# Kernel optimization log

Hardware: AMD Instinct MI355X
Metric: run time of the kernel (lower is better)

## Reference

```python
import jax, jax.numpy as jnp
import numpy as np


def _conv2d(x, w, stride, padding):
    # x: NCHW, w: OIHW
    return jax.lax.conv_general_dilated(
        x, w, window_strides=(stride, stride),
        padding=((padding, padding), (padding, padding)),
        dimension_numbers=('NCHW', 'OIHW', 'NCHW'))


def setup_inputs() -> dict:
    key = jax.random.key(0)
    k1, k2 = jax.random.split(key)
    B, C_in, H, Wd = 8, 64, 256, 256
    C_out, ksz = 64, 3
    x = jax.random.normal(k1, (B, C_in, H, Wd), dtype=jnp.float32)
    W = jax.random.normal(k2, (C_out, C_in, ksz, ksz), dtype=jnp.float32)
    b = jnp.zeros((C_out,), dtype=jnp.float32)
    return {"x": x, "W": W, "b": b}


def reference(x, W, b):
    stride, padding = 1, 1
    B, C, H, Wd = x.shape
    # per-pixel (across-channel) normalization of activations
    xf = jnp.transpose(x, (0, 2, 3, 1)).reshape(-1, C)       # [B*H*W, C]
    mu = jnp.mean(xf, axis=-1, keepdims=True)
    var = jnp.mean((xf - mu) ** 2, axis=-1, keepdims=True)    # unbiased=False
    r = 1.0 / jnp.sqrt(var + 1e-8)
    y_norm = r * (xf - mu)
    # int8 fake-quant per pixel
    s_act = 127.0 / jnp.maximum(jnp.max(jnp.abs(y_norm), axis=-1, keepdims=True), 1e-8)
    y_tilde = jnp.clip(jnp.round(s_act * y_norm), -128.0, 127.0) / s_act
    y4 = jnp.transpose(y_tilde.reshape(B, H, Wd, C), (0, 3, 1, 2))
    # ternary weight quant (value; STE only matters for backward)
    s_w = 1.0 / jnp.maximum(jnp.mean(jnp.abs(W)), 1e-8)
    w_tilde = jnp.clip(jnp.round(s_w * W), -1.0, 1.0) / s_w
    out = _conv2d(y4, w_tilde, stride, padding) + b[None, :, None, None]
    return out
```

## Files before the change

### kernel.cpp

```cpp
#include <hip/hip_runtime.h>
#include <hip/hip_bf16.h>

typedef _Float16 half8 __attribute__((ext_vector_type(8)));
typedef float    f32x4 __attribute__((ext_vector_type(4)));

#define NB   8
#define NC   64
#define NH   256
#define NW   256
#define NO   64
#define Y_OFF    0ull
#define Y_BYTES  (33554432ull * 2ull)
#define TW_OFF   (Y_OFF + Y_BYTES)
#define TW_BYTES (576ull * 64ull * 2ull)
#define MSW_OFF  (TW_OFF + TW_BYTES)

__global__ __launch_bounds__(256) void wq_kernel(const float* __restrict__ W,
                                                 _Float16* __restrict__ tw2,
                                                 float* __restrict__ msw_out) {
    __shared__ float red[256];
    __shared__ float sw_sh;
    int tid = threadIdx.x;
    float s = 0.0f;
    #pragma unroll
    for (int i = 0; i < 144; ++i) s += fabsf(W[i * 256 + tid]);
    red[tid] = s;
    __syncthreads();
    for (int off = 128; off > 0; off >>= 1) {
        if (tid < off) red[tid] += red[tid + off];
        __syncthreads();
    }
    if (tid == 0) {
        float mean = red[0] / 36864.0f;
        float msw  = fmaxf(mean, 1e-8f);
        sw_sh      = 1.0f / msw;
        msw_out[0] = msw;
    }
    __syncthreads();
    float s_w = sw_sh;
    #pragma unroll
    for (int i = 0; i < 144; ++i) {
        int idx = i * 256 + tid;
        float t = rintf(s_w * W[idx]);
        t = fminf(1.0f, fmaxf(-1.0f, t));
        int o  = idx / 576;
        int r  = idx - o * 576;
        int c  = r / 9;
        int r2 = r - c * 9;
        int kh = r2 / 3;
        int kw = r2 - kh * 3;
        int k  = (kh * 3 + kw) * 64 + c;
        tw2[((k >> 3) * 64 + o) * 8 + (k & 7)] = (_Float16)t;
    }
}

__global__ __launch_bounds__(256, 2) void norm_kernel(const float* __restrict__ x,
                                                      _Float16* __restrict__ y) {
    int p  = blockIdx.x * 256 + threadIdx.x;
    int bb = p >> 16;
    int hw = p & 65535;
    const float* xp = x + (size_t)bb * 64 * 65536 + hw;

    float v[64];
    float s = 0.0f;
    #pragma unroll
    for (int c = 0; c < 64; ++c) { v[c] = xp[(size_t)c * 65536]; s += v[c]; }
    float mu = s * (1.0f / 64.0f);

    float var = 0.0f, dmax = 0.0f;
    #pragma unroll
    for (int c = 0; c < 64; ++c) {
        float d = v[c] - mu;
        var += d * d;
        dmax = fmaxf(dmax, fabsf(d));
    }
    var *= (1.0f / 64.0f);
    float r    = 1.0f / sqrtf(var + 1e-8f);
    float amax = fmaxf(dmax * r, 1e-8f);
    float s_a  = 127.0f / amax;
    float invs = amax / 127.0f;

    half8 hv[8];
    #pragma unroll
    for (int c = 0; c < 64; ++c) {
        float yn = (v[c] - mu) * r;
        float q  = rintf(s_a * yn);
        q = fminf(127.0f, fmaxf(-128.0f, q));
        hv[c >> 3][c & 7] = (_Float16)(q * invs);
    }
    half8* yp = (half8*)(y + (size_t)p * 64);
    #pragma unroll
    for (int j = 0; j < 8; ++j) yp[j] = hv[j];
}

__global__ __launch_bounds__(256, 2) void conv_kernel(const _Float16* __restrict__ y,
                                                      const _Float16* __restrict__ tw2,
                                                      const float* __restrict__ msw_p,
                                                      const float* __restrict__ bias,
                                                      float* __restrict__ out) {
    __shared__ alignas(16) _Float16 lds[3 * 8 * 66 * 8];

    int tid = threadIdx.x;
    int bid = blockIdx.x;
    int wt = bid & 3;
    int h  = (bid >> 2) & 255;
    int bb = bid >> 10;
    int w0 = wt * 64;

    for (int i = tid; i < 1584; i += 256) {
        int cc = i & 7;
        int t8 = i >> 3;
        int wl = t8 % 66;
        int kh = t8 / 66;
        int hp = h + kh - 1;
        int wp = w0 + wl - 1;
        half8 val;
        #pragma unroll
        for (int e = 0; e < 8; ++e) val[e] = (_Float16)0.0f;
        if ((unsigned)hp < 256u && (unsigned)wp < 256u)
            val = *(const half8*)(y + ((((size_t)bb * 256 + hp) * 256 + wp) * 64 + cc * 8));
        *(half8*)(lds + ((kh * 8 + cc) * 66 + wl) * 8) = val;
    }

    int l   = tid & 63;
    int wv  = tid >> 6;
    int l15 = l & 15;
    int q8  = l >> 4;

    half8 aw[18];
    #pragma unroll
    for (int ks = 0; ks < 18; ++ks)
        aw[ks] = *(const half8*)(tw2 + (((ks * 4 + q8) * 64) + wv * 16 + l15) * 8);

    __syncthreads();

    f32x4 acc[4];
    #pragma unroll
    for (int nt = 0; nt < 4; ++nt)
        #pragma unroll
        for (int r2 = 0; r2 < 4; ++r2) acc[nt][r2] = 0.0f;

    #pragma unroll
    for (int ks = 0; ks < 18; ++ks) {
        int tap = ks >> 1;
        int kh  = tap / 3;
        int kw  = tap - kh * 3;
        int ccb = (ks & 1) * 4 + q8;
        int base = ((kh * 8 + ccb) * 66 + kw + l15) * 8;
        #pragma unroll
        for (int nt = 0; nt < 4; ++nt) {
            half8 bf = *(const half8*)(lds + base + nt * 128);
            acc[nt] = __builtin_amdgcn_mfma_f32_16x16x32_f16(aw[ks], bf, acc[nt], 0, 0, 0);
        }
    }

    float msw = *msw_p;
    size_t obase = ((size_t)bb * 64) * 65536 + (size_t)h * 256;
    #pragma unroll
    for (int reg = 0; reg < 4; ++reg) {
        int o = wv * 16 + q8 * 4 + reg;
        float bo = bias[o];
        #pragma unroll
        for (int nt = 0; nt < 4; ++nt) {
            int w = w0 + nt * 16 + l15;
            out[obase + (size_t)o * 65536 + w] = acc[nt][reg] * msw + bo;
        }
    }
}

extern "C" void kernel_launch(void* const* d_in, const int* in_sizes, int n_in,
                              void* d_out, int out_size, void* d_ws, size_t ws_size,
                              hipStream_t stream) {
    const float* x = (const float*)d_in[0];
    const float* W = (const float*)d_in[1];
    const float* b = (const float*)d_in[2];
    float* out = (float*)d_out;

    char* ws = (char*)d_ws;
    _Float16* y   = (_Float16*)(ws + Y_OFF);
    _Float16* tw2 = (_Float16*)(ws + TW_OFF);
    float*    msw = (float*)(ws + MSW_OFF);

    wq_kernel<<<1, 256, 0, stream>>>(W, tw2, msw);
    norm_kernel<<<2048, 256, 0, stream>>>(x, y);
    conv_kernel<<<8192, 256, 0, stream>>>(y, tw2, msw, b, out);
}
```

Before: 315.9 us.

## Compute four output rows per conv block to reuse halo and weight tiles

Each conv block now produces a 4-row by 64-column tile instead of a single row. The input halo grows from 3 to 6 rows shared across the 4 output rows, and each wave holds weights for 32 output channels so each LDS B-fragment feeds two MFMAs. The LDS layout changes to a pixel-major layout padded to 66 halfs per pixel to reduce bank conflicts. The goal is less redundant halo reloading and fewer LDS reads per MFMA, in exchange for more registers (doubled weight fragments and accumulators) and a quarter as many blocks.

```diff
diff --git a/kernel.cpp b/kernel.cpp
--- a/kernel.cpp
+++ b/kernel.cpp
@@ -4,11 +4,6 @@
 typedef _Float16 half8 __attribute__((ext_vector_type(8)));
 typedef float    f32x4 __attribute__((ext_vector_type(4)));
 
-#define NB   8
-#define NC   64
-#define NH   256
-#define NW   256
-#define NO   64
 #define Y_OFF    0ull
 #define Y_BYTES  (33554432ull * 2ull)
 #define TW_OFF   (Y_OFF + Y_BYTES)
@@ -93,77 +88,96 @@
     for (int j = 0; j < 8; ++j) yp[j] = hv[j];
 }
 
+#define CPAD 66
 __global__ __launch_bounds__(256, 2) void conv_kernel(const _Float16* __restrict__ y,
                                                       const _Float16* __restrict__ tw2,
                                                       const float* __restrict__ msw_p,
                                                       const float* __restrict__ bias,
                                                       float* __restrict__ out) {
-    __shared__ alignas(16) _Float16 lds[3 * 8 * 66 * 8];
+    __shared__ alignas(16) _Float16 lds[6 * 66 * CPAD];
 
     int tid = threadIdx.x;
     int bid = blockIdx.x;
     int wt = bid & 3;
-    int h  = (bid >> 2) & 255;
-    int bb = bid >> 10;
+    int hb = (bid >> 2) & 63;
+    int bb = bid >> 8;
     int w0 = wt * 64;
-
-    for (int i = tid; i < 1584; i += 256) {
+    int h0 = hb * 4;
+
+    for (int i = tid; i < 3168; i += 256) {
         int cc = i & 7;
         int t8 = i >> 3;
         int wl = t8 % 66;
-        int kh = t8 / 66;
-        int hp = h + kh - 1;
+        int r  = t8 / 66;
+        int hp = h0 + r - 1;
         int wp = w0 + wl - 1;
         half8 val;
         #pragma unroll
         for (int e = 0; e < 8; ++e) val[e] = (_Float16)0.0f;
         if ((unsigned)hp < 256u && (unsigned)wp < 256u)
             val = *(const half8*)(y + ((((size_t)bb * 256 + hp) * 256 + wp) * 64 + cc * 8));
-        *(half8*)(lds + ((kh * 8 + cc) * 66 + wl) * 8) = val;
+        *(half8*)(lds + (r * 66 + wl) * CPAD + cc * 8) = val;
     }
 
     int l   = tid & 63;
     int wv  = tid >> 6;
     int l15 = l & 15;
     int q8  = l >> 4;
-
-    half8 aw[18];
+    int oh  = wv & 1;
+    int rg  = wv >> 1;
+
+    half8 aw[18][2];
     #pragma unroll
     for (int ks = 0; ks < 18; ++ks)
-        aw[ks] = *(const half8*)(tw2 + (((ks * 4 + q8) * 64) + wv * 16 + l15) * 8);
+        #pragma unroll
+        for (int ot = 0; ot < 2; ++ot)
+            aw[ks][ot] = *(const half8*)(tw2 + (((ks * 4 + q8) * 64) + oh * 32 + ot * 16 + l15) * 8);
 
     __syncthreads();
 
-    f32x4 acc[4];
-    #pragma unroll
-    for (int nt = 0; nt < 4; ++nt)
-        #pragma unroll
-        for (int r2 = 0; r2 < 4; ++r2) acc[nt][r2] = 0.0f;
-
-    #pragma unroll
-    for (int ks = 0; ks < 18; ++ks) {
-        int tap = ks >> 1;
-        int kh  = tap / 3;
-        int kw  = tap - kh * 3;
-        int ccb = (ks & 1) * 4 + q8;
-        int base = ((kh * 8 + ccb) * 66 + kw + l15) * 8;
-        #pragma unroll
-        for (int nt = 0; nt < 4; ++nt) {
-            half8 bf = *(const half8*)(lds + base + nt * 128);
-            acc[nt] = __builtin_amdgcn_mfma_f32_16x16x32_f16(aw[ks], bf, acc[nt], 0, 0, 0);
+    float msw = *msw_p;
+    #pragma unroll
+    for (int rr = 0; rr < 2; ++rr) {
+        f32x4 acc[2][4];
+        #pragma unroll
+        for (int ot = 0; ot < 2; ++ot)
+            #pragma unroll
+            for (int nt = 0; nt < 4; ++nt)
+                #pragma unroll
+                for (int e = 0; e < 4; ++e) acc[ot][nt][e] = 0.0f;
+
+        int rloc = rg * 2 + rr;
+
+        #pragma unroll
+        for (int ks = 0; ks < 18; ++ks) {
+            int tap = ks >> 1;
+            int kh  = tap / 3;
+            int kw  = tap - kh * 3;
+            int cbase = (ks & 1) * 32 + q8 * 8;
+            const _Float16* lrow = lds + ((rloc + kh) * 66 + kw + l15) * CPAD + cbase;
+            #pragma unroll
+            for (int nt = 0; nt < 4; ++nt) {
+                half8 bf = *(const half8*)(lrow + nt * 16 * CPAD);
+                #pragma unroll
+                for (int ot = 0; ot < 2; ++ot)
+                    acc[ot][nt] = __builtin_amdgcn_mfma_f32_16x16x32_f16(aw[ks][ot], bf, acc[ot][nt], 0, 0, 0);
+            }
         }
-    }
-
-    float msw = *msw_p;
-    size_t obase = ((size_t)bb * 64) * 65536 + (size_t)h * 256;
-    #pragma unroll
-    for (int reg = 0; reg < 4; ++reg) {
-        int o = wv * 16 + q8 * 4 + reg;
-        float bo = bias[o];
-        #pragma unroll
-        for (int nt = 0; nt < 4; ++nt) {
-            int w = w0 + nt * 16 + l15;
-            out[obase + (size_t)o * 65536 + w] = acc[nt][reg] * msw + bo;
+
+        int hout = h0 + rloc;
+        size_t obase = ((size_t)bb * 64) * 65536 + (size_t)hout * 256;
+        #pragma unroll
+        for (int ot = 0; ot < 2; ++ot) {
+            #pragma unroll
+            for (int reg = 0; reg < 4; ++reg) {
+                int o = oh * 32 + ot * 16 + q8 * 4 + reg;
+                float bo = bias[o];
+                #pragma unroll
+                for (int nt = 0; nt < 4; ++nt) {
+                    int w = w0 + nt * 16 + l15;
+                    out[obase + (size_t)o * 65536 + w] = acc[ot][nt][reg] * msw + bo;
+                }
+            }
         }
     }
 }
@@ -183,5 +197,5 @@
 
     wq_kernel<<<1, 256, 0, stream>>>(W, tw2, msw);
     norm_kernel<<<2048, 256, 0, stream>>>(x, y);
-    conv_kernel<<<8192, 256, 0, stream>>>(y, tw2, msw, b, out);
-}
+    conv_kernel<<<2048, 256, 0, stream>>>(y, tw2, msw, b, out);
+}
```

Measured after the change: 404.4 us. 28.0% more time.
